# Kernel tuning notes

Measured on AMD Instinct MI355X. Metric: run time of the kernel, lower is better.

Reference implementation:

```python
import jax, jax.numpy as jnp
import numpy as np
import math

T, HW, M, D, DK, H, SIGMA = 16, 1024, 256, 768, 768, 8, 0.5
HD = DK // H
VHD = D // H
EPS = 1e-6
SCALE = 1.0 / math.sqrt(HD)


def _ln(x, g):
    # LayerNorm(eps=1e-6, bias=False)
    m = x.mean(-1, keepdims=True)
    v = ((x - m) ** 2).mean(-1, keepdims=True)
    return (x - m) / jnp.sqrt(v + EPS) * g


def setup_inputs() -> dict:
    key = jax.random.key(0)
    ks = jax.random.split(key, 16)
    s = 0.02
    features = jax.random.normal(ks[0], (T, HW, D), jnp.float32)
    tracks = jax.random.uniform(ks[1], (T, M, 2), jnp.float32)
    track_pos_embeddings = jax.random.normal(ks[2], (T, M, D), jnp.float32)
    feature_pos_embeddings = jax.random.normal(ks[3], (T, HW, D), jnp.float32)
    g = jnp.linspace(0.0, 1.0, 32)
    feature_positions = jnp.stack(jnp.meshgrid(g, g, indexing='ij'), axis=-1).reshape(HW, 2)
    return {
        'features': features,
        'tracks': tracks,
        'feature_positions': feature_positions,
        'track_pos_embeddings': track_pos_embeddings,
        'feature_pos_embeddings': feature_pos_embeddings,
        # AttentionalSampling params (nn.Linear weights are [out,in])
        'Wq_s': jax.random.normal(ks[4], (DK, D)) * s,
        'Wk_s': jax.random.normal(ks[5], (DK, D)) * s,
        'Wv_s': jax.random.normal(ks[6], (D, D)) * s,
        'qg_s': jnp.ones((DK,), jnp.float32),
        'kg_s': jnp.ones((DK,), jnp.float32),
        'Wo_s': jax.random.normal(ks[7], (D, D)) * s,
        # AttentionalSplatting params
        'Wq_p': jax.random.normal(ks[8], (DK, D)) * s,
        'Wk_p': jax.random.normal(ks[9], (DK, D)) * s,
        'Wv_p': jax.random.normal(ks[10], (D, D)) * s,
        'qg_p': jnp.ones((DK,), jnp.float32),
        'kg_p': jnp.ones((DK,), jnp.float32),
        'Wout_p': jax.random.normal(ks[11], (D, D)) * s,
    }


def reference(features, tracks, feature_positions, track_pos_embeddings,
              feature_pos_embeddings, Wq_s, Wk_s, Wv_s, qg_s, kg_s, Wo_s,
              Wq_p, Wk_p, Wv_p, qg_p, kg_p, Wout_p):
    # per-frame Gaussian spatial bias from squared euclidean distances
    # d2[t,m,n] = ||tracks[t,m] - feature_positions[n]||^2  -> [T, M, HW]
    d2 = ((tracks[:, :, None, :] - feature_positions[None, None, :, :]) ** 2).sum(-1)
    bias = -d2 / (2.0 * SIGMA ** 2)  # [T, M, HW]

    # ---- Attentional Sampling: tracks query features ----
    Q = _ln(track_pos_embeddings @ Wq_s.T, qg_s)          # [T, M, DK]
    K = _ln((features + feature_pos_embeddings) @ Wk_s.T, kg_s)  # [T, HW, DK]
    V = features @ Wv_s.T                                  # [T, HW, D]
    Qh = Q.reshape(T, M, H, HD).transpose(0, 2, 1, 3)      # [T, H, M, HD]
    Kh = K.reshape(T, HW, H, HD).transpose(0, 2, 1, 3)     # [T, H, HW, HD]
    Vh = V.reshape(T, HW, H, VHD).transpose(0, 2, 1, 3)    # [T, H, HW, VHD]
    scores = jnp.einsum('thmd,thnd->thmn', Qh, Kh) * SCALE + bias[:, None]
    A = jax.nn.softmax(scores, axis=-1)
    sampled = jnp.einsum('thmn,thnd->thmd', A, Vh)
    sampled = sampled.transpose(0, 2, 1, 3).reshape(T, M, D) @ Wo_s.T  # [T, M, D]

    # ---- Attentional Splatting: features query tracks ----
    Q2 = _ln(feature_pos_embeddings @ Wq_p.T, qg_p)        # [T, HW, DK]
    K2 = _ln(track_pos_embeddings @ Wk_p.T, kg_p)          # [T, M, DK]
    V2 = sampled @ Wv_p.T                                   # [T, M, D]
    Q2h = Q2.reshape(T, HW, H, HD).transpose(0, 2, 1, 3)   # [T, H, HW, HD]
    K2h = K2.reshape(T, M, H, HD).transpose(0, 2, 1, 3)    # [T, H, M, HD]
    V2h = V2.reshape(T, M, H, VHD).transpose(0, 2, 1, 3)   # [T, H, M, VHD]
    bias_t = jnp.swapaxes(bias, 1, 2)                       # [T, HW, M] (cdist is symmetric)
    scores2 = jnp.einsum('thnd,thmd->thnm', Q2h, K2h) * SCALE + bias_t[:, None]
    A2 = jax.nn.softmax(scores2, axis=-1)
    upd = jnp.einsum('thnm,thmd->thnd', A2, V2h)
    feature_updates = upd.transpose(0, 2, 1, 3).reshape(T, HW, D) @ Wout_p.T
    return features + feature_updates
```

## Files before the change

kernel.cpp:

```cpp
#include <hip/hip_runtime.h>

#define DD 768
#define HDIM 96
#define ATT_SCALE 0.10206207261596575f

typedef float floatx4 __attribute__((ext_vector_type(4)));
typedef __bf16 bf16;
typedef bf16 bf16x8 __attribute__((ext_vector_type(8)));
typedef bf16 bf16x4 __attribute__((ext_vector_type(4)));
typedef bf16 bf16x2 __attribute__((ext_vector_type(2)));

__device__ __forceinline__ void gl2lds16(const bf16* g, bf16* l) {
  __builtin_amdgcn_global_load_lds(
      (const __attribute__((address_space(1))) void*)g,
      (__attribute__((address_space(3))) void*)l, 16, 0, 0);
}

__global__ __launch_bounds__(256) void prep(
    const float* __restrict__ features, const float* __restrict__ fpe,
    const float* __restrict__ tpe,
    const float* w0, const float* w1, const float* w2, const float* w3,
    const float* w4, const float* w5, const float* w6, const float* w7,
    bf16* __restrict__ Fb, bf16* __restrict__ Xb, bf16* __restrict__ Feb,
    bf16* __restrict__ Tb, bf16* __restrict__ Wb, bf16* __restrict__ WoT) {
  const int b = blockIdx.x;
  const int tid = threadIdx.x;
  if (b < 6144) {
    const int i = (b * 256 + tid) * 8;
    floatx4 f0 = *(const floatx4*)(features + i);
    floatx4 f1 = *(const floatx4*)(features + i + 4);
    floatx4 e0 = *(const floatx4*)(fpe + i);
    floatx4 e1 = *(const floatx4*)(fpe + i + 4);
    bf16x8 fv, xv, ev;
#pragma unroll
    for (int k = 0; k < 4; k++) {
      fv[k] = (bf16)f0[k];           fv[k + 4] = (bf16)f1[k];
      ev[k] = (bf16)e0[k];           ev[k + 4] = (bf16)e1[k];
      xv[k] = (bf16)(f0[k] + e0[k]); xv[k + 4] = (bf16)(f1[k] + e1[k]);
    }
    *(bf16x8*)(Fb + i) = fv;
    *(bf16x8*)(Xb + i) = xv;
    *(bf16x8*)(Feb + i) = ev;
  } else if (b < 7680) {
    const int i = ((b - 6144) * 256 + tid) * 8;
    floatx4 s0 = *(const floatx4*)(tpe + i);
    floatx4 s1 = *(const floatx4*)(tpe + i + 4);
    bf16x8 v;
#pragma unroll
    for (int k = 0; k < 4; k++) { v[k] = (bf16)s0[k]; v[k + 4] = (bf16)s1[k]; }
    *(bf16x8*)(Tb + i) = v;
  } else if (b < 9984) {
    const int sub = b - 7680;
    const int wi = sub / 288, xb = sub % 288;
    const float* srcs[8] = {w0, w1, w2, w3, w4, w5, w6, w7};
    const float* s = srcs[wi];
    bf16* d = Wb + (size_t)wi * 589824;
    const int i = (xb * 256 + tid) * 8;
    floatx4 s0 = *(const floatx4*)(s + i);
    floatx4 s1 = *(const floatx4*)(s + i + 4);
    bf16x8 v;
#pragma unroll
    for (int k = 0; k < 4; k++) { v[k] = (bf16)s0[k]; v[k + 4] = (bf16)s1[k]; }
    *(bf16x8*)(d + i) = v;
  } else {
    __shared__ float Ts[64][65];
    const int sub = b - 9984;
    const int X0 = (sub % 12) * 64, Y0 = (sub / 12) * 64;
    const int r = tid >> 2;
    const int c4 = (tid & 3) * 16;
    const float* src = w3 + (size_t)(Y0 + r) * DD + X0 + c4;
#pragma unroll
    for (int k = 0; k < 16; k += 4) {
      floatx4 v = *(const floatx4*)(src + k);
      Ts[r][c4 + k] = v[0]; Ts[r][c4 + k + 1] = v[1];
      Ts[r][c4 + k + 2] = v[2]; Ts[r][c4 + k + 3] = v[3];
    }
    __syncthreads();
    bf16 o[16];
#pragma unroll
    for (int k = 0; k < 16; k++) o[k] = (bf16)Ts[c4 + k][r];
    *(bf16x8*)(WoT + (size_t)(X0 + r) * DD + Y0 + c4) = *(bf16x8*)&o[0];
    *(bf16x8*)(WoT + (size_t)(X0 + r) * DD + Y0 + c4 + 8) = *(bf16x8*)&o[8];
  }
}

__device__ __forceinline__ void ln_row(bf16* x, const float* g, int lane) {
  float v[12], s = 0.f, ss = 0.f;
#pragma unroll
  for (int j = 0; j < 3; j++) {
    bf16x4 b = *(const bf16x4*)&x[j * 256 + lane * 4];
#pragma unroll
    for (int e = 0; e < 4; e++) {
      float t = (float)b[e];
      v[j * 4 + e] = t; s += t; ss += t * t;
    }
  }
#pragma unroll
  for (int o = 32; o > 0; o >>= 1) { s += __shfl_xor(s, o); ss += __shfl_xor(ss, o); }
  const float mean = s * (1.0f / DD);
  const float inv = rsqrtf(ss * (1.0f / DD) - mean * mean + 1e-6f);
#pragma unroll
  for (int j = 0; j < 3; j++) {
    floatx4 gg = *(const floatx4*)&g[j * 256 + lane * 4];
    bf16x4 o4;
#pragma unroll
    for (int e = 0; e < 4; e++) o4[e] = (bf16)((v[j * 4 + e] - mean) * inv * gg[e]);
    *(bf16x4*)&x[j * 256 + lane * 4] = o4;
  }
}

__global__ __launch_bounds__(256) void ln_all(bf16* X0, const float* g0,
                                              bf16* X1, const float* g1,
                                              bf16* X2, const float* g2,
                                              bf16* X3, const float* g3) {
  const int b = blockIdx.x;
  bf16* X; const float* g; int base;
  if (b < 4096)      { X = X0; g = g0; base = b; }
  else if (b < 8192) { X = X1; g = g1; base = b - 4096; }
  else if (b < 9216) { X = X2; g = g2; base = b - 8192; }
  else               { X = X3; g = g3; base = b - 9216; }
  const int w = threadIdx.x >> 6, lane = threadIdx.x & 63;
  ln_row(X + (size_t)(base * 4 + w) * DD, g, lane);
}

#define BAR() do { __builtin_amdgcn_sched_barrier(0); \
                   __builtin_amdgcn_s_barrier(); \
                   __builtin_amdgcn_sched_barrier(0); } while (0)
#define VMW(n) asm volatile("s_waitcnt vmcnt(" #n ")" ::: "memory")

template <int MODE>
__device__ __forceinline__ void gemm256(const bf16* __restrict__ A,
                                        const bf16* __restrict__ W,
                                        bf16* __restrict__ Cb,
                                        float* __restrict__ Cf,
                                        const float* __restrict__ addsrc,
                                        bf16* lds, int row0, int col0) {
  const int tid = threadIdx.x;
  const int lane = tid & 63;
  const int w = tid >> 6;
  const int wm = (w & 1) * 128;
  const int wn = (w >> 1) * 64;
  const int fr = lane & 15;
  const int quad = lane >> 4;
  const int f7 = fr & 7;

  const int srow = tid >> 3;
  const int sswz = ((tid & 7) ^ (srow & 7)) * 8;
  const bf16* Ag = A + (size_t)(row0 + srow) * DD + sswz;
  const bf16* Wg = W + (size_t)(col0 + srow) * DD + sswz;
  bf16* dA = lds + tid * 8;
  bf16* dB = lds + 32768 + tid * 8;

#define STGA(tau, h) do { \
    gl2lds16(Ag + (size_t)((h) * 128) * DD + (tau) * 64, \
             dA + ((tau) & 1) * 16384 + (h) * 8192); \
    gl2lds16(Ag + (size_t)((h) * 128 + 64) * DD + (tau) * 64, \
             dA + ((tau) & 1) * 16384 + (h) * 8192 + 4096); \
  } while (0)
#define STGB(tau, h) do { \
    gl2lds16(Wg + (size_t)((h) * 128) * DD + (tau) * 64, \
             dB + ((tau) & 1) * 16384 + (h) * 8192); \
    gl2lds16(Wg + (size_t)((h) * 128 + 64) * DD + (tau) * 64, \
             dB + ((tau) & 1) * 16384 + (h) * 8192 + 4096); \
  } while (0)

  const int sl0 = (quad ^ f7) * 8;
  const int sl1 = ((4 | quad) ^ f7) * 8;

#define LDA8(buf, mh) do { \
    _Pragma("unroll") for (int m = 0; m < 4; m++) { \
      const bf16* p = lds + (buf) * 16384 + (wm + (mh) * 64 + m * 16 + fr) * 64; \
      af[m][0] = *(const bf16x8*)(p + sl0); \
      af[m][1] = *(const bf16x8*)(p + sl1); } \
  } while (0)
#define LDB4(buf, nh, dst) do { \
    _Pragma("unroll") for (int n = 0; n < 2; n++) { \
      const bf16* p = lds + 32768 + (buf) * 16384 + (wn + (nh) * 32 + n * 16 + fr) * 64; \
      dst[n][0] = *(const bf16x8*)(p + sl0); \
      dst[n][1] = *(const bf16x8*)(p + sl1); } \
  } while (0)
#define MM16(mh, nbase, bb) do { \
    __builtin_amdgcn_s_setprio(1); \
    _Pragma("unroll") for (int m = 0; m < 4; m++) \
    _Pragma("unroll") for (int n = 0; n < 2; n++) { \
      acc[(mh) * 4 + m][(nbase) + n] = __builtin_amdgcn_mfma_f32_16x16x32_bf16( \
          af[m][0], bb[n][0], acc[(mh) * 4 + m][(nbase) + n], 0, 0, 0); \
      acc[(mh) * 4 + m][(nbase) + n] = __builtin_amdgcn_mfma_f32_16x16x32_bf16( \
          af[m][1], bb[n][1], acc[(mh) * 4 + m][(nbase) + n], 0, 0, 0); } \
    __builtin_amdgcn_s_setprio(0); \
  } while (0)

  floatx4 acc[8][4];

  STGB(0, 0); STGB(0, 1); STGA(0, 0); STGA(0, 1);
  STGB(1, 0); STGB(1, 1);
#pragma unroll
  for (int i = 0; i < 8; i++)
#pragma unroll
    for (int j = 0; j < 4; j++) acc[i][j] = (floatx4){0, 0, 0, 0};
  VMW(4);
  BAR();

  bf16x8 af[4][2], b0[2][2], b1[2][2];

  for (int it = 0; it < 6; ++it) {
    const int a = 2 * it;
    const bool stg = (it < 5);
    LDA8(0, 0); LDB4(0, 0, b0);
    STGA(a + 1, 0);
    BAR();
    MM16(0, 0, b0);
    BAR();
    LDB4(0, 1, b1);
    STGA(a + 1, 1);
    BAR();
    MM16(0, 2, b1);
    BAR();
    LDA8(0, 1);
    if (stg) STGB(a + 2, 0);
    BAR();
    MM16(1, 2, b1);
    BAR();
    if (stg) STGB(a + 2, 1);
    BAR();
    MM16(1, 0, b0);
    if (stg) { VMW(4); } else { VMW(0); }
    BAR();
    LDA8(1, 0); LDB4(1, 0, b0);
    if (stg) STGA(a + 2, 0);
    BAR();
    MM16(0, 0, b0);
    BAR();
    LDB4(1, 1, b1);
    if (stg) STGA(a + 2, 1);
    BAR();
    MM16(0, 2, b1);
    BAR();
    LDA8(1, 1);
    if (stg) STGB(a + 3, 0);
    BAR();
    MM16(1, 2, b1);
    BAR();
    if (stg) STGB(a + 3, 1);
    BAR();
    MM16(1, 0, b0);
    if (stg) VMW(4);
    BAR();
  }

#pragma unroll
  for (int m = 0; m < 8; m++)
#pragma unroll
    for (int n = 0; n < 4; n++)
#pragma unroll
      for (int r = 0; r < 4; r++) {
        const int row = row0 + wm + m * 16 + quad * 4 + r;
        const int col = col0 + wn + n * 16 + fr;
        const size_t idx = (size_t)row * DD + col;
        if (MODE == 0) Cb[idx] = (bf16)acc[m][n][r];
        else Cf[idx] = acc[m][n][r] + addsrc[idx];
      }
#undef STGA
#undef STGB
#undef LDA8
#undef LDB4
#undef MM16
}

__global__ __launch_bounds__(512, 2) void gemm_all(
    const bf16* Xb, const bf16* Fb, const bf16* Feb, const bf16* Tb,
    const bf16* Wb, const bf16* WoT,
    bf16* Kc, bf16* Vc, bf16* Qb2, bf16* Qc, bf16* K2, bf16* Wcr) {
  __shared__ bf16 lds[65536];
  const size_t SW = (size_t)768 * 768;
  const int z = blockIdx.z;
  if (z == 0)
    gemm256<0>(Xb, Wb + 1 * SW, Kc, nullptr, nullptr, lds,
               blockIdx.x * 256, blockIdx.y * 256);
  else if (z == 1)
    gemm256<0>(Fb, Wb + 2 * SW, Vc, nullptr, nullptr, lds,
               blockIdx.x * 256, blockIdx.y * 256);
  else if (z == 2)
    gemm256<0>(Feb, Wb + 4 * SW, Qb2, nullptr, nullptr, lds,
               blockIdx.x * 256, blockIdx.y * 256);
  else {
    const int x = blockIdx.x;
    if (x < 16)
      gemm256<0>(Tb, Wb + 0 * SW, Qc, nullptr, nullptr, lds,
                 x * 256, blockIdx.y * 256);
    else if (x < 32)
      gemm256<0>(Tb, Wb + 5 * SW, K2, nullptr, nullptr, lds,
                 (x - 16) * 256, blockIdx.y * 256);
    else if (x < 35)
      gemm256<0>(Wb + 6 * SW, WoT, Wcr, nullptr, nullptr, lds,
                 (x - 32) * 256, blockIdx.y * 256);
  }
}

__global__ __launch_bounds__(512, 2) void gemm_b(const bf16* A, const bf16* W, bf16* C) {
  __shared__ bf16 lds[65536];
  gemm256<0>(A, W, C, nullptr, nullptr, lds, blockIdx.x * 256, blockIdx.y * 256);
}

__global__ __launch_bounds__(512, 2) void gemm_final(const bf16* A, const bf16* W,
                                                     float* C, const float* addsrc) {
  __shared__ bf16 lds[65536];
  gemm256<1>(A, W, nullptr, C, addsrc, lds, blockIdx.x * 256, blockIdx.y * 256);
}

template <int SPLIT>
__global__ __launch_bounds__(512, 4) void attn512(
    const bf16* __restrict__ Qb, const bf16* __restrict__ Kb,
    const bf16* __restrict__ Vb, bf16* __restrict__ Ob,
    float* __restrict__ Ml,
    const float* __restrict__ qpos, int qpos_ts,
    const float* __restrict__ kpos, int kpos_ts,
    int nq, int nk, int npq, int nsp) {
  const int b = blockIdx.x;
  const int h = b & 7;
  const int t = (b >> 3) & 15;
  const int rest = b >> 7;
  const int qt = rest % npq;
  const int sp = rest / npq;
  const int klen = nk / nsp;
  const int k0s = sp * klen;
  const int q0 = qt * 128;
  const bf16* Q = Qb + (size_t)t * nq * DD + h * HDIM;
  const bf16* K = Kb + (size_t)t * nk * DD + h * HDIM;
  const bf16* V = Vb + (size_t)t * nk * DD + h * HDIM;
  bf16* O = Ob + (size_t)(SPLIT ? (sp * 16 + t) : t) * nq * DD + h * HDIM;
  const float* qp = qpos + (size_t)t * qpos_ts;
  const float* kp = kpos + (size_t)t * kpos_ts;

  __shared__ bf16 Ks[64 * 104];
  __shared__ bf16 Vt[96 * 72];
  __shared__ bf16 Ps[2 * 64 * 72];

  const int tid = threadIdx.x;
  const int w = tid >> 6;
  const int g = w >> 2;
  const int wl = w & 3;
  const int lane = tid & 63;
  const int fr = lane & 15;
  const int quad = lane >> 4;
  const int rowb = wl * 16;
  const int qgb = q0 + g * 64;
  bf16* Pg = &Ps[g * 64 * 72];

  bf16x8 qf[3];
  {
    const bf16* qrow = Q + (size_t)(qgb + rowb + fr) * DD;
#pragma unroll
    for (int c = 0; c < 3; c++) qf[c] = *(const bf16x8*)(qrow + c * 32 + quad * 8);
  }
  float qx[4], qy[4];
#pragma unroll
  for (int r = 0; r < 4; r++) {
    int qi = qgb + rowb + quad * 4 + r;
    qx[r] = qp[qi * 2];
    qy[r] = qp[qi * 2 + 1];
  }

  float lrow[4] = {0.f, 0.f, 0.f, 0.f};
  floatx4 oacc[6];
#pragma unroll
  for (int d = 0; d < 6; d++) oacc[d] = (floatx4){0, 0, 0, 0};

  const int krA = tid >> 3, kcA = (tid & 7) * 8;
  const int krB = (tid & 255) >> 2, kcB = 64 + (tid & 3) * 8;
  const int nb = (tid & 31) * 2, db = (tid >> 5) * 6;

  for (int n0 = k0s; n0 < k0s + klen; n0 += 64) {
    __syncthreads();
    *(bf16x8*)&Ks[krA * 104 + kcA] =
        *(const bf16x8*)(K + (size_t)(n0 + krA) * DD + kcA);
    if (tid < 256)
      *(bf16x8*)&Ks[krB * 104 + kcB] =
          *(const bf16x8*)(K + (size_t)(n0 + krB) * DD + kcB);
    {
      bf16 tmp[2][6];
#pragma unroll
      for (int nn = 0; nn < 2; nn++) {
        const unsigned* vg = (const unsigned*)(V + (size_t)(n0 + nb + nn) * DD + db);
        unsigned u0 = vg[0], u1 = vg[1], u2 = vg[2];
        *(unsigned*)&tmp[nn][0] = u0;
        *(unsigned*)&tmp[nn][2] = u1;
        *(unsigned*)&tmp[nn][4] = u2;
      }
#pragma unroll
      for (int dd = 0; dd < 6; dd++) {
        bf16x2 v2 = {tmp[0][dd], tmp[1][dd]};
        *(bf16x2*)&Vt[(db + dd) * 72 + nb] = v2;
      }
    }
    __syncthreads();

    floatx4 s4[4];
#pragma unroll
    for (int j = 0; j < 4; j++) {
      floatx4 sa = {0, 0, 0, 0};
#pragma unroll
      for (int c = 0; c < 3; c++) {
        bf16x8 kf = *(const bf16x8*)&Ks[(j * 16 + fr) * 104 + c * 32 + quad * 8];
        sa = __builtin_amdgcn_mfma_f32_16x16x32_bf16(qf[c], kf, sa, 0, 0, 0);
      }
      s4[j] = sa;
    }
    float kxx[4], kyy[4];
#pragma unroll
    for (int j = 0; j < 4; j++) {
      int ki = (n0 + j * 16 + fr) * 2;
      kxx[j] = kp[ki];
      kyy[j] = kp[ki + 1];
    }
#pragma unroll
    for (int j = 0; j < 4; j++)
#pragma unroll
      for (int r = 0; r < 4; r++) {
        float dx = qx[r] - kxx[j], dy = qy[r] - kyy[j];
        float sv = s4[j][r] * ATT_SCALE - 2.0f * (dx * dx + dy * dy);
        float pv = __expf(sv);
        lrow[r] += pv;
        Pg[(rowb + quad * 4 + r) * 72 + j * 16 + fr] = (bf16)pv;
      }
    bf16x8 pf0 = *(const bf16x8*)&Pg[(rowb + fr) * 72 + quad * 8];
    bf16x8 pf1 = *(const bf16x8*)&Pg[(rowb + fr) * 72 + 32 + quad * 8];
#pragma unroll
    for (int d = 0; d < 6; d++) {
      bf16x8 v0 = *(const bf16x8*)&Vt[(d * 16 + fr) * 72 + quad * 8];
      bf16x8 v1 = *(const bf16x8*)&Vt[(d * 16 + fr) * 72 + 32 + quad * 8];
      oacc[d] = __builtin_amdgcn_mfma_f32_16x16x32_bf16(pf0, v0, oacc[d], 0, 0, 0);
      oacc[d] = __builtin_amdgcn_mfma_f32_16x16x32_bf16(pf1, v1, oacc[d], 0, 0, 0);
    }
  }

#pragma unroll
  for (int r = 0; r < 4; r++)
#pragma unroll
    for (int o = 1; o < 16; o <<= 1) lrow[r] += __shfl_xor(lrow[r], o);

#pragma unroll
  for (int r = 0; r < 4; r++) {
    int row = qgb + rowb + quad * 4 + r;
    if (SPLIT) {
#pragma unroll
      for (int d = 0; d < 6; d++)
        O[(size_t)row * DD + d * 16 + fr] = (bf16)oacc[d][r];
      if (fr == 0)
        Ml[((size_t)(sp * 16 + t) * 8 + h) * nq + row] = lrow[r];
    } else {
      float inv = 1.0f / lrow[r];
#pragma unroll
      for (int d = 0; d < 6; d++)
        O[(size_t)row * DD + d * 16 + fr] = (bf16)(oacc[d][r] * inv);
    }
  }
}

__global__ __launch_bounds__(256) void combine4(const bf16* __restrict__ Op,
                                                const float* __restrict__ Ml,
                                                bf16* __restrict__ Out) {
  const int row = blockIdx.x;
  const int t = row >> 8;
  const int q = row & 255;
#pragma unroll
  for (int e = 0; e < 3; e++) {
    int dim = threadIdx.x + e * 256;
    int hh = dim / 96;
    float osum = 0.f, lsum = 0.f;
#pragma unroll
    for (int s = 0; s < 4; s++) {
      lsum += Ml[((size_t)(s * 16 + t) * 8 + hh) * 256 + q];
      osum += (float)Op[((size_t)(s * 16 + t) * 256 + q) * DD + dim];
    }
    Out[(size_t)row * DD + dim] = (bf16)(osum / lsum);
  }
}

extern "C" void kernel_launch(void* const* d_in, const int* in_sizes, int n_in,
                              void* d_out, int out_size, void* d_ws, size_t ws_size,
                              hipStream_t stream) {
  const float* features = (const float*)d_in[0];
  const float* tracks   = (const float*)d_in[1];
  const float* fpos     = (const float*)d_in[2];
  const float* tpe      = (const float*)d_in[3];
  const float* fpe      = (const float*)d_in[4];
  const float* Wq_s     = (const float*)d_in[5];
  const float* Wk_s     = (const float*)d_in[6];
  const float* Wv_s     = (const float*)d_in[7];
  const float* qg_s     = (const float*)d_in[8];
  const float* kg_s     = (const float*)d_in[9];
  const float* Wo_s     = (const float*)d_in[10];
  const float* Wq_p     = (const float*)d_in[11];
  const float* Wk_p     = (const float*)d_in[12];
  const float* Wv_p     = (const float*)d_in[13];
  const float* qg_p     = (const float*)d_in[14];
  const float* kg_p     = (const float*)d_in[15];
  const float* Wout_p   = (const float*)d_in[16];
  float* out = (float*)d_out;

  const size_t SB = (size_t)16 * 1024 * 768;
  const size_t SS = (size_t)16 * 256 * 768;
  const size_t SW = (size_t)768 * 768;
  bf16* p = (bf16*)d_ws;
  bf16* Fb  = p; p += SB;
  bf16* Xb  = p; p += SB;
  bf16* Feb = p; p += SB;
  bf16* Kc  = p; p += SB;
  bf16* Vc  = p; p += SB;
  bf16* Qb2 = p; p += SB;
  bf16* Tb  = p; p += SS;
  bf16* Qc  = p; p += SS;
  bf16* K2  = p; p += SS;
  bf16* Sh  = p; p += SS;
  bf16* Op  = p; p += 4 * SS;
  bf16* Wb  = p; p += 8 * SW;
  bf16* WoT = p; p += SW;
  bf16* Wcr = p; p += SW;
  float* Ml = (float*)p;
  bf16* V2 = Qc; bf16* U = Fb;

  dim3 blk(256);

  prep<<<10128, blk, 0, stream>>>(features, fpe, tpe,
                                  Wq_s, Wk_s, Wv_s, Wo_s, Wq_p, Wk_p, Wv_p, Wout_p,
                                  Fb, Xb, Feb, Tb, Wb, WoT);
  gemm_all<<<dim3(64, 3, 4), dim3(512), 0, stream>>>(Xb, Fb, Feb, Tb, Wb, WoT,
                                                     Kc, Vc, Qb2, Qc, K2, Wcr);
  ln_all<<<10240, blk, 0, stream>>>(Kc, kg_s, Qb2, qg_p, Qc, qg_s, K2, kg_p);
  attn512<1><<<1024, dim3(512), 0, stream>>>(Qc, Kc, Vc, Op, Ml,
                                             tracks, 512, fpos, 0, 256, 1024, 2, 4);
  combine4<<<4096, blk, 0, stream>>>(Op, Ml, Sh);
  gemm_b<<<dim3(16, 3), dim3(512), 0, stream>>>(Sh, Wcr, V2);
  attn512<0><<<1024, dim3(512), 0, stream>>>(Qb2, K2, V2, U, nullptr,
                                             fpos, 0, tracks, 512, 1024, 256, 8, 1);
  gemm_final<<<dim3(64, 3), dim3(512), 0, stream>>>(U, Wb + 7 * SW, out, features);
}
```

Baseline: 440.1 us.

## Prefetch next K/V tile into registers while computing current attention tile

Restructures the attention key loop into a register double-buffered pipeline. The next tile's K and V global loads are issued before computing the current tile, so memory latency overlaps with MFMA work. Key positions are also staged once into LDS (Kpl) instead of being read from global memory every iteration. This adds register pressure from the two register buffer sets. Kpl holds 512 floats, which assumes klen is at most 256.

Result: no change. 436.5 us (-0.8%).

```diff
diff --git a/kernel.cpp b/kernel.cpp
--- a/kernel.cpp
+++ b/kernel.cpp
@@ -335,6 +335,7 @@
   __shared__ bf16 Ks[64 * 104];
   __shared__ bf16 Vt[96 * 72];
   __shared__ bf16 Ps[2 * 64 * 72];
+  __shared__ float Kpl[512];
 
   const int tid = threadIdx.x;
   const int w = tid >> 6;
@@ -370,31 +371,33 @@
   const int krB = (tid & 255) >> 2, kcB = 64 + (tid & 3) * 8;
   const int nb = (tid & 31) * 2, db = (tid >> 5) * 6;
 
-  for (int n0 = k0s; n0 < k0s + klen; n0 += 64) {
-    __syncthreads();
-    *(bf16x8*)&Ks[krA * 104 + kcA] =
-        *(const bf16x8*)(K + (size_t)(n0 + krA) * DD + kcA);
-    if (tid < 256)
-      *(bf16x8*)&Ks[krB * 104 + kcB] =
-          *(const bf16x8*)(K + (size_t)(n0 + krB) * DD + kcB);
-    {
-      bf16 tmp[2][6];
-#pragma unroll
-      for (int nn = 0; nn < 2; nn++) {
-        const unsigned* vg = (const unsigned*)(V + (size_t)(n0 + nb + nn) * DD + db);
-        unsigned u0 = vg[0], u1 = vg[1], u2 = vg[2];
-        *(unsigned*)&tmp[nn][0] = u0;
-        *(unsigned*)&tmp[nn][2] = u1;
-        *(unsigned*)&tmp[nn][4] = u2;
-      }
-#pragma unroll
-      for (int dd = 0; dd < 6; dd++) {
-        bf16x2 v2 = {tmp[0][dd], tmp[1][dd]};
-        *(bf16x2*)&Vt[(db + dd) * 72 + nb] = v2;
-      }
-    }
-    __syncthreads();
-
+  Kpl[tid] = kp[(size_t)k0s * 2 + tid];
+
+  struct VR { unsigned a, b, c; };
+  bf16x8 kaA, kbA, kaB, kbB;
+  VR vA0, vA1, vB0, vB1;
+
+  auto loadreg = [&](int n0, bf16x8& ka, bf16x8& kb, VR& r0, VR& r1) {
+    ka = *(const bf16x8*)(K + (size_t)(n0 + krA) * DD + kcA);
+    if (tid < 256) kb = *(const bf16x8*)(K + (size_t)(n0 + krB) * DD + kcB);
+    const unsigned* g0 = (const unsigned*)(V + (size_t)(n0 + nb) * DD + db);
+    const unsigned* g1 = (const unsigned*)(V + (size_t)(n0 + nb + 1) * DD + db);
+    r0.a = g0[0]; r0.b = g0[1]; r0.c = g0[2];
+    r1.a = g1[0]; r1.b = g1[1]; r1.c = g1[2];
+  };
+  auto writelds = [&](const bf16x8& ka, const bf16x8& kb, const VR& r0, const VR& r1) {
+    *(bf16x8*)&Ks[krA * 104 + kcA] = ka;
+    if (tid < 256) *(bf16x8*)&Ks[krB * 104 + kcB] = kb;
+    bf16 t0[6], t1[6];
+    *(unsigned*)&t0[0] = r0.a; *(unsigned*)&t0[2] = r0.b; *(unsigned*)&t0[4] = r0.c;
+    *(unsigned*)&t1[0] = r1.a; *(unsigned*)&t1[2] = r1.b; *(unsigned*)&t1[4] = r1.c;
+#pragma unroll
+    for (int dd = 0; dd < 6; dd++) {
+      bf16x2 v2 = {t0[dd], t1[dd]};
+      *(bf16x2*)&Vt[(db + dd) * 72 + nb] = v2;
+    }
+  };
+  auto compute = [&](int rel) {
     floatx4 s4[4];
 #pragma unroll
     for (int j = 0; j < 4; j++) {
@@ -409,9 +412,9 @@
     float kxx[4], kyy[4];
 #pragma unroll
     for (int j = 0; j < 4; j++) {
-      int ki = (n0 + j * 16 + fr) * 2;
-      kxx[j] = kp[ki];
-      kyy[j] = kp[ki + 1];
+      int ki = (rel + j * 16 + fr) * 2;
+      kxx[j] = Kpl[ki];
+      kyy[j] = Kpl[ki + 1];
     }
 #pragma unroll
     for (int j = 0; j < 4; j++)
@@ -432,6 +435,22 @@
       oacc[d] = __builtin_amdgcn_mfma_f32_16x16x32_bf16(pf0, v0, oacc[d], 0, 0, 0);
       oacc[d] = __builtin_amdgcn_mfma_f32_16x16x32_bf16(pf1, v1, oacc[d], 0, 0, 0);
     }
+  };
+
+  const int NT = klen >> 6;
+  loadreg(k0s, kaA, kbA, vA0, vA1);
+  for (int n = 0; n < NT; n += 2) {
+    __syncthreads();
+    writelds(kaA, kbA, vA0, vA1);
+    if (n + 1 < NT) loadreg(k0s + (n + 1) * 64, kaB, kbB, vB0, vB1);
+    __syncthreads();
+    compute(n * 64);
+    if (n + 1 >= NT) break;
+    __syncthreads();
+    writelds(kaB, kbB, vB0, vB1);
+    if (n + 2 < NT) loadreg(k0s + (n + 2) * 64, kaA, kbA, vA0, vA1);
+    __syncthreads();
+    compute((n + 1) * 64);
   }
 
 #pragma unroll
```
